# Kernel optimization log

Measured on AMD Instinct MI355X. Metric: run time of the kernel, lower is better.

## Reference

```python
import jax, jax.numpy as jnp
import numpy as np

EPS = 1e-08
STEPS_START = 0
STEPS_END = 500


def setup_inputs() -> dict:
    key = jax.random.key(0)
    k_x, k_w, k_beta, k_b = jax.random.split(key, 4)
    B, T, D_in, D_out = 64, 500, 1024, 128
    x = jax.random.normal(k_x, (B, T, D_in), dtype=jnp.float32)
    # w ~ N(w_init_mean, w_init_std * sqrt(1/input_shape))
    w = jax.random.normal(k_w, (D_in, D_out), dtype=jnp.float32) * np.sqrt(1.0 / D_in)
    beta = jax.random.uniform(k_beta, (D_out,), dtype=jnp.float32)  # clamped to [0,1] in torch
    b = jax.random.uniform(k_b, (D_out,), dtype=jnp.float32)        # clamped >= 0 in torch
    return {"x": x, "w": w, "beta": beta, "b": b}


def reference(x, w, beta, b):
    # x: [B, T, D_in], w: [D_in, D_out], beta/b: [D_out]
    h = jnp.einsum('btc,cd->btd', x, w)          # [B, T, D_out]
    norm = jnp.sum(w * w, axis=0)                # [D_out]

    one_minus_beta = 1.0 - beta

    def step(mem, h_t):
        mem = mem * beta + one_minus_beta * h_t  # Leaky_Neuron=True
        return mem, mem

    mem0 = jnp.zeros((x.shape[0], w.shape[1]), dtype=x.dtype)
    _, mem_rec = jax.lax.scan(step, mem0, jnp.swapaxes(h, 0, 1))  # [T, B, D_out]
    mem_rec = jnp.swapaxes(mem_rec, 0, 1)                          # [B, T, D_out]

    # time_reduction == 'mean'
    output = jnp.mean(mem_rec[:, STEPS_START:STEPS_END, :], axis=1) / (norm + EPS) - b
    return output
```

## Files before the change

### kernel.cpp

```cpp
#include <hip/hip_runtime.h>
#include <hip/hip_bf16.h>

#define B_    64
#define T_    500
#define DIN   1024
#define DOUT  128
#define EPSV  1e-8f
#define BM    128
#define BK    64
#define NKC   2
#define KCL   (DIN / NKC)
#define NKT   (KCL / BK)
#define TILES 4

typedef __attribute__((ext_vector_type(8))) short bf16x8;
typedef __attribute__((ext_vector_type(4))) float f32x4;

#define OFF_WTAB  262144
#define OFF_SCALE 518144
#define OFF_PART  518656

__device__ inline short f2bf(float f) {
    __hip_bfloat16 h = __float2bfloat16(f);
    return __builtin_bit_cast(short, h);
}

__device__ inline void block_sync_lds() {
    asm volatile("s_waitcnt lgkmcnt(0)" ::: "memory");
    __builtin_amdgcn_s_barrier();
    asm volatile("" ::: "memory");
}

__global__ __launch_bounds__(256) void prep_kernel(
    const float* __restrict__ w, const float* __restrict__ beta,
    __hip_bfloat16* __restrict__ wT, float* __restrict__ wtab,
    float* __restrict__ scale)
{
    int bid = blockIdx.x, tid = threadIdx.x;
    if (bid < 512) {
        int i = bid * 256 + tid;
        int d = i >> 10, k = i & 1023;
        wT[(size_t)d * DIN + k] = __float2bfloat16(w[(size_t)k * DOUT + d]);
    } else if (bid < 640) {
        int d = bid - 512;
        __shared__ float red[256];
        float s = 0.f;
        for (int c = tid; c < DIN; c += 256) {
            float v = w[(size_t)c * DOUT + d];
            s += v * v;
        }
        red[tid] = s;
        __syncthreads();
        for (int off = 128; off > 0; off >>= 1) {
            if (tid < off) red[tid] += red[tid + off];
            __syncthreads();
        }
        if (tid == 0) scale[d] = 1.f / ((red[0] + EPSV) * (float)T_);
    } else {
        int i = (bid - 640) * 256 + tid;
        if (i < T_ * DOUT) {
            int t = i >> 7, d = i & 127;
            wtab[i] = 1.f - powf(beta[d], (float)(T_ - t));
        }
    }
}

__global__ __launch_bounds__(512, 4) void gemm_kernel(
    const float* __restrict__ x, const __hip_bfloat16* __restrict__ wT,
    const float* __restrict__ wtab, float* __restrict__ partials)
{
    __shared__ __align__(16) char smem[2 * 32768];

    const int wg   = blockIdx.x;
    const int kc   = wg & 1;
    const int tile = (wg >> 1) & 3;
    const int b    = wg >> 3;
    const int t0   = tile * BM;
    const int kbase = kc * KCL;
    const int tid  = threadIdx.x;
    const int wid  = tid >> 6;
    const int lane = tid & 63;
    const int arow = lane & 15;
    const int kblk = lane >> 4;
    const int wr   = wid >> 2;
    const int wc   = wid & 3;

    const float* xb = x + (size_t)b * T_ * DIN + kbase;

    const int sr = tid >> 4;
    const int sc = tid & 15;
    const float* ag[4];
    int awoff[4];
#pragma unroll
    for (int p = 0; p < 4; ++p) {
        int row  = p * 32 + sr;
        int trow = t0 + row; if (trow >= T_) trow = T_ - 1;
        ag[p] = xb + (size_t)trow * DIN + sc * 4;
        awoff[p] = (row * 128 + sc * 8) ^ ((row & 7) << 4);
    }
    const int bcol = tid >> 2;
    const int bch0 = (tid & 3) * 2;
    const __hip_bfloat16* bg0 = wT + (size_t)bcol * DIN + kbase + bch0 * 8;
    const __hip_bfloat16* bg1 = bg0 + 8;
    const int bwoff0 = (bcol * 128 + bch0 * 16)        ^ ((bcol & 7) << 4);
    const int bwoff1 = (bcol * 128 + (bch0 + 1) * 16)  ^ ((bcol & 7) << 4);

    int aro[4][2], bro[2][2];
#pragma unroll
    for (int fm = 0; fm < 4; ++fm)
#pragma unroll
        for (int kk = 0; kk < 2; ++kk) {
            int row = wr * 64 + fm * 16 + arow;
            aro[fm][kk] = (row * 128 + kk * 64 + kblk * 16) ^ ((row & 7) << 4);
        }
#pragma unroll
    for (int fn = 0; fn < 2; ++fn)
#pragma unroll
        for (int kk = 0; kk < 2; ++kk) {
            int col = wc * 32 + fn * 16 + arow;
            bro[fn][kk] = (col * 128 + kk * 64 + kblk * 16) ^ ((col & 7) << 4);
        }

    f32x4 acc[4][2] = {};

#define DECL_SET(S) float4 S##a0, S##a1, S##a2, S##a3; bf16x8 S##b0, S##b1;
#define LOAD_SET(S, KB) \
    S##a0 = *reinterpret_cast<const float4*>(ag[0] + (KB)); \
    S##a1 = *reinterpret_cast<const float4*>(ag[1] + (KB)); \
    S##a2 = *reinterpret_cast<const float4*>(ag[2] + (KB)); \
    S##a3 = *reinterpret_cast<const float4*>(ag[3] + (KB)); \
    S##b0 = *reinterpret_cast<const bf16x8*>(bg0 + (KB));   \
    S##b1 = *reinterpret_cast<const bf16x8*>(bg1 + (KB));
#define WRITE_SET(S, AB, BB) { \
    short4 h0; h0.x=f2bf(S##a0.x); h0.y=f2bf(S##a0.y); h0.z=f2bf(S##a0.z); h0.w=f2bf(S##a0.w); \
    *reinterpret_cast<short4*>((AB) + awoff[0]) = h0; \
    short4 h1; h1.x=f2bf(S##a1.x); h1.y=f2bf(S##a1.y); h1.z=f2bf(S##a1.z); h1.w=f2bf(S##a1.w); \
    *reinterpret_cast<short4*>((AB) + awoff[1]) = h1; \
    short4 h2; h2.x=f2bf(S##a2.x); h2.y=f2bf(S##a2.y); h2.z=f2bf(S##a2.z); h2.w=f2bf(S##a2.w); \
    *reinterpret_cast<short4*>((AB) + awoff[2]) = h2; \
    short4 h3; h3.x=f2bf(S##a3.x); h3.y=f2bf(S##a3.y); h3.z=f2bf(S##a3.z); h3.w=f2bf(S##a3.w); \
    *reinterpret_cast<short4*>((AB) + awoff[3]) = h3; \
    *reinterpret_cast<bf16x8*>((BB) + bwoff0) = S##b0; \
    *reinterpret_cast<bf16x8*>((BB) + bwoff1) = S##b1; }
#define COMPUTE(AB, BB) { \
    _Pragma("unroll") \
    for (int kk = 0; kk < 2; ++kk) { \
        bf16x8 bf0 = *reinterpret_cast<const bf16x8*>((BB) + bro[0][kk]); \
        bf16x8 bf1 = *reinterpret_cast<const bf16x8*>((BB) + bro[1][kk]); \
        _Pragma("unroll") \
        for (int fm = 0; fm < 4; ++fm) { \
            bf16x8 af = *reinterpret_cast<const bf16x8*>((AB) + aro[fm][kk]); \
            acc[fm][0] = __builtin_amdgcn_mfma_f32_16x16x32_bf16(af, bf0, acc[fm][0], 0, 0, 0); \
            acc[fm][1] = __builtin_amdgcn_mfma_f32_16x16x32_bf16(af, bf1, acc[fm][1], 0, 0, 0); \
        } } }

    DECL_SET(qe_)
    DECL_SET(qo_)

    LOAD_SET(qe_, 0)
    LOAD_SET(qo_, BK)
    WRITE_SET(qe_, smem, smem + 16384)
    block_sync_lds();

#pragma unroll
    for (int kt = 0; kt < NKT; ++kt) {
        char* Acur = smem + (kt & 1) * 32768;
        char* Bcur = Acur + 16384;
        char* Anxt = smem + ((kt + 1) & 1) * 32768;
        char* Bnxt = Anxt + 16384;

        if (kt + 2 < NKT) {
            if (kt & 1) { LOAD_SET(qo_, (kt + 2) * BK) }
            else        { LOAD_SET(qe_, (kt + 2) * BK) }
        }

        COMPUTE(Acur, Bcur)

        if (kt + 1 < NKT) {
            if (kt & 1) { WRITE_SET(qe_, Anxt, Bnxt) }
            else        { WRITE_SET(qo_, Anxt, Bnxt) }
            block_sync_lds();
        }
    }
#undef DECL_SET
#undef LOAD_SET
#undef WRITE_SET
#undef COMPUTE

    const int col0 = wc * 32 + arow;
    const int col1 = col0 + 16;
    float s0 = 0.f, s1 = 0.f;
#pragma unroll
    for (int fm = 0; fm < 4; ++fm) {
#pragma unroll
        for (int r = 0; r < 4; ++r) {
            int t = t0 + wr * 64 + fm * 16 + kblk * 4 + r;
            if (t < T_) {
                s0 += wtab[t * DOUT + col0] * acc[fm][0][r];
                s1 += wtab[t * DOUT + col1] * acc[fm][1][r];
            }
        }
    }
    s0 += __shfl_xor(s0, 16); s0 += __shfl_xor(s0, 32);
    s1 += __shfl_xor(s1, 16); s1 += __shfl_xor(s1, 32);

    if (kblk == 0) {
        float* p = partials + ((((size_t)b * TILES + tile) * 2 + wr) * NKC + kc) * DOUT;
        p[col0] = s0;
        p[col1] = s1;
    }
}

__global__ __launch_bounds__(256) void finalize_kernel(
    const float* __restrict__ partials, const float* __restrict__ scale,
    const float* __restrict__ bias, float* __restrict__ out)
{
    int i = blockIdx.x * 256 + threadIdx.x;
    int b = i >> 7, d = i & 127;
    float s = 0.f;
#pragma unroll
    for (int p = 0; p < TILES * 2 * NKC; ++p)
        s += partials[((size_t)b * TILES * 2 * NKC + p) * DOUT + d];
    out[i] = s * scale[d] - bias[d];
}

extern "C" void kernel_launch(void* const* d_in, const int* in_sizes, int n_in,
                              void* d_out, int out_size, void* d_ws, size_t ws_size,
                              hipStream_t stream) {
    const float* x    = (const float*)d_in[0];
    const float* w    = (const float*)d_in[1];
    const float* beta = (const float*)d_in[2];
    const float* bias = (const float*)d_in[3];
    float* out = (float*)d_out;

    char* ws = (char*)d_ws;
    __hip_bfloat16* wT = (__hip_bfloat16*)(ws);
    float* wtab     = (float*)(ws + OFF_WTAB);
    float* scale    = (float*)(ws + OFF_SCALE);
    float* partials = (float*)(ws + OFF_PART);

    prep_kernel<<<890, 256, 0, stream>>>(w, beta, wT, wtab, scale);
    gemm_kernel<<<B_ * TILES * NKC, 512, 0, stream>>>(x, wT, wtab, partials);
    finalize_kernel<<<(B_ * DOUT) / 256, 256, 0, stream>>>(partials, scale, bias, out);
}
```

Before: 34.66 us.

## Drop decay-weight table, compute weights inline, move norm into GEMM launch

Removes the precomputed per-(t,d) table of 1 - beta^(T-t) weights and recomputes them in the GEMM epilogue with exp2f of a per-column log2(beta). The column-norm reduction moves out of the prep kernel into 16 extra workgroups of the GEMM launch, each using wave shuffles. The weight transpose now writes 8 bf16 values per thread with a vector store. The aim is a lighter prep kernel and no table traffic, at the cost of transcendental math in the epilogue and a slightly different float rounding of the decay weights.

```diff
diff --git a/kernel.cpp b/kernel.cpp
--- a/kernel.cpp
+++ b/kernel.cpp
@@ -12,13 +12,14 @@
 #define KCL   (DIN / NKC)
 #define NKT   (KCL / BK)
 #define TILES 4
+#define NGEMM (B_ * TILES * NKC)
+#define NNORM 16
 
 typedef __attribute__((ext_vector_type(8))) short bf16x8;
 typedef __attribute__((ext_vector_type(4))) float f32x4;
 
-#define OFF_WTAB  262144
-#define OFF_SCALE 518144
-#define OFF_PART  518656
+#define OFF_SCALE 262144
+#define OFF_PART  262656
 
 __device__ inline short f2bf(float f) {
     __hip_bfloat16 h = __float2bfloat16(f);
@@ -31,44 +32,45 @@
     asm volatile("" ::: "memory");
 }
 
-__global__ __launch_bounds__(256) void prep_kernel(
-    const float* __restrict__ w, const float* __restrict__ beta,
-    __hip_bfloat16* __restrict__ wT, float* __restrict__ wtab,
-    float* __restrict__ scale)
+__global__ __launch_bounds__(512) void prep_kernel(
+    const float* __restrict__ w, __hip_bfloat16* __restrict__ wT)
 {
-    int bid = blockIdx.x, tid = threadIdx.x;
-    if (bid < 512) {
-        int i = bid * 256 + tid;
-        int d = i >> 10, k = i & 1023;
-        wT[(size_t)d * DIN + k] = __float2bfloat16(w[(size_t)k * DOUT + d]);
-    } else if (bid < 640) {
-        int d = bid - 512;
-        __shared__ float red[256];
+    int t  = blockIdx.x * 512 + threadIdx.x;
+    int d  = t & 127;
+    int kq = t >> 7;
+    float v[8];
+#pragma unroll
+    for (int m = 0; m < 8; ++m)
+        v[m] = w[(size_t)(kq * 8 + m) * DOUT + d];
+    bf16x8 o;
+#pragma unroll
+    for (int m = 0; m < 8; ++m) o[m] = f2bf(v[m]);
+    *reinterpret_cast<bf16x8*>(wT + (size_t)d * DIN + kq * 8) = o;
+}
+
+__global__ __launch_bounds__(512, 4) void gemm_kernel(
+    const float* __restrict__ x, const float* __restrict__ w,
+    const float* __restrict__ beta, const __hip_bfloat16* __restrict__ wT,
+    float* __restrict__ partials, float* __restrict__ scale)
+{
+    const int tid  = threadIdx.x;
+    const int wid  = tid >> 6;
+    const int lane = tid & 63;
+
+    if (blockIdx.x >= NGEMM) {
+        int d = (blockIdx.x - NGEMM) * 8 + wid;
         float s = 0.f;
-        for (int c = tid; c < DIN; c += 256) {
-            float v = w[(size_t)c * DOUT + d];
+#pragma unroll
+        for (int i = 0; i < 16; ++i) {
+            float v = w[(size_t)(lane + 64 * i) * DOUT + d];
             s += v * v;
         }
-        red[tid] = s;
-        __syncthreads();
-        for (int off = 128; off > 0; off >>= 1) {
-            if (tid < off) red[tid] += red[tid + off];
-            __syncthreads();
-        }
-        if (tid == 0) scale[d] = 1.f / ((red[0] + EPSV) * (float)T_);
-    } else {
-        int i = (bid - 640) * 256 + tid;
-        if (i < T_ * DOUT) {
-            int t = i >> 7, d = i & 127;
-            wtab[i] = 1.f - powf(beta[d], (float)(T_ - t));
-        }
-    }
-}
-
-__global__ __launch_bounds__(512, 4) void gemm_kernel(
-    const float* __restrict__ x, const __hip_bfloat16* __restrict__ wT,
-    const float* __restrict__ wtab, float* __restrict__ partials)
-{
+        s += __shfl_xor(s, 1);  s += __shfl_xor(s, 2);  s += __shfl_xor(s, 4);
+        s += __shfl_xor(s, 8);  s += __shfl_xor(s, 16); s += __shfl_xor(s, 32);
+        if (lane == 0) scale[d] = 1.f / ((s + EPSV) * (float)T_);
+        return;
+    }
+
     __shared__ __align__(16) char smem[2 * 32768];
 
     const int wg   = blockIdx.x;
@@ -77,9 +79,6 @@
     const int b    = wg >> 3;
     const int t0   = tile * BM;
     const int kbase = kc * KCL;
-    const int tid  = threadIdx.x;
-    const int wid  = tid >> 6;
-    const int lane = tid & 63;
     const int arow = lane & 15;
     const int kblk = lane >> 4;
     const int wr   = wid >> 2;
@@ -189,6 +188,8 @@
 
     const int col0 = wc * 32 + arow;
     const int col1 = col0 + 16;
+    const float lb0 = log2f(beta[col0]);
+    const float lb1 = log2f(beta[col1]);
     float s0 = 0.f, s1 = 0.f;
 #pragma unroll
     for (int fm = 0; fm < 4; ++fm) {
@@ -196,8 +197,9 @@
         for (int r = 0; r < 4; ++r) {
             int t = t0 + wr * 64 + fm * 16 + kblk * 4 + r;
             if (t < T_) {
-                s0 += wtab[t * DOUT + col0] * acc[fm][0][r];
-                s1 += wtab[t * DOUT + col1] * acc[fm][1][r];
+                float e = (float)(T_ - t);
+                s0 += (1.f - exp2f(e * lb0)) * acc[fm][0][r];
+                s1 += (1.f - exp2f(e * lb1)) * acc[fm][1][r];
             }
         }
     }
@@ -235,11 +237,10 @@
 
     char* ws = (char*)d_ws;
     __hip_bfloat16* wT = (__hip_bfloat16*)(ws);
-    float* wtab     = (float*)(ws + OFF_WTAB);
     float* scale    = (float*)(ws + OFF_SCALE);
     float* partials = (float*)(ws + OFF_PART);
 
-    prep_kernel<<<890, 256, 0, stream>>>(w, beta, wT, wtab, scale);
-    gemm_kernel<<<B_ * TILES * NKC, 512, 0, stream>>>(x, wT, wtab, partials);
+    prep_kernel<<<32, 512, 0, stream>>>(w, wT);
+    gemm_kernel<<<NGEMM + NNORM, 512, 0, stream>>>(x, w, beta, wT, partials, scale);
     finalize_kernel<<<(B_ * DOUT) / 256, 256, 0, stream>>>(partials, scale, bias, out);
 }
```

Measured after the change: 35.82 us. +3.4%, slower.
